# Optimization experiments

Hardware: AMD Instinct MI355X
Metric: run time of the kernel (lower is better)

Reference implementation:

```python
import jax, jax.numpy as jnp
import numpy as np

Nw, Nt, IN_DIM, OUT_DIM, H, FEAT = 200000, 20000, 128, 256, 8, 64
DH = OUT_DIM // H
DEG = 32
E = Nt * DEG
FFN = 512
NEG_SLOPE = 0.01  # F.leaky_relu default


def setup_inputs() -> dict:
    key = jax.random.key(0)
    ks = jax.random.split(key, 12)
    w = jax.random.normal(ks[0], (Nw, IN_DIM), jnp.float32)
    t = jax.random.normal(ks[1], (Nt, OUT_DIM), jnp.float32)
    topic_feat = jax.random.normal(ks[2], (Nt, FEAT), jnp.float32)
    edge_src = jax.random.randint(ks[3], (E,), 0, Nw)
    # every topic node gets exactly DEG in-edges (sorted dst, no empty segments)
    edge_dst = jnp.repeat(jnp.arange(Nt), DEG)
    s = lambda k, sh, f: jax.random.normal(k, sh, jnp.float32) * np.float32(f)
    fc_w = s(ks[4], (H, IN_DIM, DH), 1.0 / np.sqrt(IN_DIM))
    attn_a = s(ks[5], (H, 2 * DH), 1.0 / np.sqrt(2 * DH))
    dstfeat_w = s(ks[6], (H, FEAT, DH), 1.0 / np.sqrt(FEAT))
    proj_w = s(ks[7], (2 * OUT_DIM, OUT_DIM), 1.0 / np.sqrt(2 * OUT_DIM))
    proj_b = jnp.zeros((OUT_DIM,), jnp.float32)
    ffn_w1 = s(ks[8], (OUT_DIM, FFN), 1.0 / np.sqrt(OUT_DIM))
    ffn_b1 = jnp.zeros((FFN,), jnp.float32)
    ffn_w2 = s(ks[9], (FFN, OUT_DIM), 1.0 / np.sqrt(FFN))
    ffn_b2 = jnp.zeros((OUT_DIM,), jnp.float32)
    ln_scale = jnp.ones((OUT_DIM,), jnp.float32)
    ln_bias = jnp.zeros((OUT_DIM,), jnp.float32)
    return dict(w=w, t=t, topic_feat=topic_feat, edge_src=edge_src, edge_dst=edge_dst,
                fc_w=fc_w, attn_a=attn_a, dstfeat_w=dstfeat_w, proj_w=proj_w, proj_b=proj_b,
                ffn_w1=ffn_w1, ffn_b1=ffn_b1, ffn_w2=ffn_w2, ffn_b2=ffn_b2,
                ln_scale=ln_scale, ln_bias=ln_bias)


def reference(w, t, topic_feat, edge_src, edge_dst, fc_w, attn_a, dstfeat_w,
              proj_w, proj_b, ffn_w1, ffn_b1, ffn_w2, ffn_b2, ln_scale, ln_bias):
    # per-head projections: z on word (src) nodes, dstfeat on topic (dst) nodes
    z = jnp.einsum('ni,hid->hnd', w, fc_w)              # [H, Nw, DH]
    dz = jnp.einsum('nf,hfd->hnd', topic_feat, dstfeat_w)  # [H, Nt, DH]
    # attn_fc(cat(z_src, dstfeat)) decomposes into per-node dot products
    s_src = jnp.einsum('hnd,hd->hn', z, attn_a[:, :DH])   # [H, Nw]
    s_dst = jnp.einsum('hnd,hd->hn', dz, attn_a[:, DH:])  # [H, Nt]
    e = s_src[:, edge_src] + s_dst[:, edge_dst]           # [H, E]
    e = jnp.where(e >= 0, e, NEG_SLOPE * e)               # leaky_relu
    # segment softmax over incoming edges of each dst node (DGL mailbox softmax)
    seg_max = jax.vmap(lambda v: jax.ops.segment_max(v, edge_dst, num_segments=Nt))(e)
    seg_max = jnp.where(jnp.isfinite(seg_max), seg_max, 0.0)  # guard empty segments
    p = jnp.exp(e - seg_max[:, edge_dst])
    denom = jax.vmap(lambda v: jax.ops.segment_sum(v, edge_dst, num_segments=Nt))(p)
    alpha = p / jnp.maximum(denom[:, edge_dst], 1e-9)     # [H, E]
    msg = alpha[:, :, None] * z[:, edge_src, :]           # [H, E, DH]
    agg = jax.vmap(lambda m: jax.ops.segment_sum(m, edge_dst, num_segments=Nt))(msg)  # [H, Nt, DH]
    h = jnp.transpose(agg, (1, 0, 2)).reshape(Nt, OUT_DIM)  # head concat
    h = jax.nn.elu(h)
    h = jnp.concatenate([h, t], axis=-1) @ proj_w + proj_b  # [Nt, OUT_DIM]
    # PositionwiseFeedForward: LN -> gelu -> linear -> residual (dropout off in eval)
    mu = jnp.mean(h, axis=-1, keepdims=True)
    var = jnp.var(h, axis=-1, keepdims=True)
    xn = (h - mu) / jnp.sqrt(var + 1e-6) * ln_scale + ln_bias
    inter = jax.nn.gelu(xn @ ffn_w1 + ffn_b1, approximate=False)
    return (inter @ ffn_w2 + ffn_b2) + h
```

## Files before the change

### kernel.cpp

```cpp
#include <hip/hip_runtime.h>
#include <hip/hip_bf16.h>

typedef __attribute__((ext_vector_type(8))) short short8v;
typedef __attribute__((ext_vector_type(4))) float f32x4;

#define NW 200000
#define NT 20000
#define KIN 128
#define ODIM 256
#define NH 8
#define DH_ 32
#define FEAT_ 64
#define DEG_ 32
#define FFN_ 512

#define WS_Z     0ull
#define WS_SSRC  102400000ull
#define WS_SDST  108800000ull
#define WS_TBF   119680000ull
#define WS_B1T   129920000ull
#define WS_PWT   129985536ull
#define WS_W1T   130247680ull
#define WS_W2T   130509824ull
#define WS_ABT   130771968ull


__device__ __forceinline__ unsigned short f2bf(float x) {
    __hip_bfloat16 b = __float2bfloat16(x);
    return *reinterpret_cast<unsigned short*>(&b);
}
__device__ __forceinline__ float bf2f(unsigned short u) {
    unsigned int v = ((unsigned int)u) << 16;
    return __uint_as_float(v);
}

__global__ __launch_bounds__(256) void prep_w(const float* __restrict__ fc_w,
        const float* __restrict__ proj_w, const float* __restrict__ w1,
        const float* __restrict__ w2, const float* __restrict__ attn_a,
        unsigned short* __restrict__ b1f, unsigned short* __restrict__ pwf,
        unsigned short* __restrict__ w1f, unsigned short* __restrict__ w2f,
        unsigned short* __restrict__ abt) {
    int i = blockIdx.x * 256 + threadIdx.x;
    int j = i & 7, l = (i >> 3) & 63;
    int l16 = l & 15, lq = l >> 4;
    if (i < 32768) {
        int kk = (i >> 9) & 3, g = i >> 11;
        int c = g * 16 + l16, k = kk * 32 + lq * 8 + j;
        int h = c >> 5, d = c & 31;
        b1f[i] = f2bf(fc_w[(h * KIN + k) * DH_ + d]);
    }
    if (i < 4096) {
        int h = i >> 8, p = i & 255;
        int c = (p >> 6) * 64 + (p & 3) * 16 + ((p >> 2) & 15);
        abt[i] = ((c >> 5) == h) ? f2bf(attn_a[h * 64 + (c & 31)]) : (unsigned short)0;
    }
    {
        int kk = (i >> 9) & 15, g = i >> 13;
        int c = g * 16 + l16, k = kk * 32 + lq * 8 + j;
        int kp = k;
        if (k < 256)
            kp = ((k >> 6) << 6) + (k & 3) * 16 + ((k >> 2) & 15);
        pwf[i] = f2bf(proj_w[(size_t)kp * ODIM + c]);
    }
    {
        int kk = (i >> 9) & 7, g = i >> 12;
        int c = g * 16 + l16, k = kk * 32 + lq * 8 + j;
        w1f[i] = f2bf(w1[(size_t)k * FFN_ + c]);
    }
    {
        int kk = (i >> 9) & 15, g = i >> 13;
        int c = g * 16 + l16, k = kk * 32 + lq * 8 + j;
        w2f[i] = f2bf(w2[(size_t)k * ODIM + c]);
    }
}

__global__ __launch_bounds__(256) void prep_t(const float* __restrict__ t,
                                              unsigned short* __restrict__ tbf) {
    int i = blockIdx.x * 256 + threadIdx.x;
    const float4* p = (const float4*)(t + (size_t)i * 8);
    float4 a = p[0], b = p[1];
    short8v o;
    o[0] = (short)f2bf(a.x); o[1] = (short)f2bf(a.y);
    o[2] = (short)f2bf(a.z); o[3] = (short)f2bf(a.w);
    o[4] = (short)f2bf(b.x); o[5] = (short)f2bf(b.y);
    o[6] = (short)f2bf(b.z); o[7] = (short)f2bf(b.w);
    *((short8v*)tbf + i) = o;
}

#define ZRP 264
#define TPB 5
__global__ __launch_bounds__(256) void k1_z(const float* __restrict__ w,
        const unsigned short* __restrict__ b1f, const unsigned short* __restrict__ abt,
        unsigned short* __restrict__ z, float* __restrict__ s_src) {
    __shared__ unsigned short aS[2][64 * 136];
    __shared__ unsigned short zR[64 * ZRP];
    const int tid = threadIdx.x;
    const int wv = tid >> 6, l = tid & 63;
    const int l16 = l & 15, lq = l >> 4;
    const int tile0 = blockIdx.x * TPB;
    float4 vb[8];
    #pragma unroll
    for (int j = 0; j < 8; ++j) {
        int i = tid + j * 256;
        int r = i >> 5, kq = i & 31;
        vb[j] = *(const float4*)(w + (size_t)(tile0 * 64 + r) * KIN + kq * 4);
    }
    #pragma unroll
    for (int j = 0; j < 8; ++j) {
        int i = tid + j * 256;
        int r = i >> 5, kq = i & 31;
        ushort4 u;
        u.x = f2bf(vb[j].x); u.y = f2bf(vb[j].y);
        u.z = f2bf(vb[j].z); u.w = f2bf(vb[j].w);
        *(ushort4*)(&aS[0][r * 136 + kq * 4]) = u;
    }
    for (int t = 0; t < TPB; ++t) {
        const int cur = t & 1;
        const int row0 = (tile0 + t) * 64;
        if (t < TPB - 1) {
            #pragma unroll
            for (int j = 0; j < 8; ++j) {
                int i = tid + j * 256;
                int r = i >> 5, kq = i & 31;
                vb[j] = *(const float4*)(w + (size_t)(row0 + 64 + r) * KIN + kq * 4);
            }
        }
        __syncthreads();
        f32x4 acc[4][4];
        #pragma unroll
        for (int a = 0; a < 4; ++a)
            #pragma unroll
            for (int b = 0; b < 4; ++b)
                acc[a][b] = (f32x4){0.f, 0.f, 0.f, 0.f};
        #pragma unroll
        for (int kk = 0; kk < 4; ++kk) {
            short8v af[4], bfr[4];
            #pragma unroll
            for (int rf = 0; rf < 4; ++rf)
                af[rf] = *(const short8v*)(&aS[cur][(rf * 16 + l16) * 136 + kk * 32 + lq * 8]);
            #pragma unroll
            for (int cf = 0; cf < 4; ++cf)
                bfr[cf] = *(const short8v*)((const short*)b1f +
                            ((((wv * 4 + cf) * 4 + kk) << 9) + l * 8));
            #pragma unroll
            for (int rf = 0; rf < 4; ++rf)
                #pragma unroll
                for (int cf = 0; cf < 4; ++cf)
                    acc[rf][cf] = __builtin_amdgcn_mfma_f32_16x16x32_bf16(
                        af[rf], bfr[cf], acc[rf][cf], 0, 0, 0);
        }
        #pragma unroll
        for (int rl = 0; rl < 4; ++rl)
            #pragma unroll
            for (int q = 0; q < 4; ++q) {
                int row = rl * 16 + lq * 4 + q;
                ushort4 u;
                u.x = f2bf(acc[rl][0][q]); u.y = f2bf(acc[rl][1][q]);
                u.z = f2bf(acc[rl][2][q]); u.w = f2bf(acc[rl][3][q]);
                *(ushort4*)(&zR[row * ZRP + wv * 64 + l16 * 4]) = u;
            }
        __syncthreads();
        {
            const int base = wv * 16;
            f32x4 sacc = (f32x4){0.f, 0.f, 0.f, 0.f};
            #pragma unroll
            for (int kk = 0; kk < 8; ++kk) {
                short8v a = *(const short8v*)(&zR[(base + l16) * ZRP + kk * 32 + lq * 8]);
                short8v b = *(const short8v*)((const short*)abt + (size_t)l16 * 256 + kk * 32 + lq * 8);
                sacc = __builtin_amdgcn_mfma_f32_16x16x32_bf16(a, b, sacc, 0, 0, 0);
            }
            if (l16 < NH) {
                #pragma unroll
                for (int q = 0; q < 4; ++q)
                    s_src[(size_t)(row0 + base + lq * 4 + q) * NH + l16] = sacc[q];
            }
        }
        #pragma unroll
        for (int j = 0; j < 8; ++j) {
            int idx = tid + j * 256;
            int r = idx >> 5, ch = idx & 31;
            short8v v = *(const short8v*)(&zR[r * ZRP + ch * 8]);
            *(short8v*)(z + (size_t)(row0 + r) * ODIM + ch * 8) = v;
        }
        if (t < TPB - 1) {
            #pragma unroll
            for (int j = 0; j < 8; ++j) {
                int i = tid + j * 256;
                int r = i >> 5, kq = i & 31;
                ushort4 u;
                u.x = f2bf(vb[j].x); u.y = f2bf(vb[j].y);
                u.z = f2bf(vb[j].z); u.w = f2bf(vb[j].w);
                *(ushort4*)(&aS[cur ^ 1][r * 136 + kq * 4]) = u;
            }
        }
    }
}

__global__ __launch_bounds__(256) void k_sdst(const float* __restrict__ topic_feat,
        const float* __restrict__ dstfeat_w, const float* __restrict__ attn_a,
        float* __restrict__ s_dst) {
    __shared__ float rS[NH * 65];
    __shared__ float tfS[32 * 65];
    const int tid = threadIdx.x;
    for (int i = tid; i < NH * FEAT_; i += 256) {
        int h = i >> 6, f = i & 63;
        const float* dw = dstfeat_w + (size_t)(h * FEAT_ + f) * DH_;
        const float* aa = attn_a + h * 64 + DH_;
        float s = 0.f;
        #pragma unroll
        for (int d = 0; d < DH_; ++d) s += dw[d] * aa[d];
        rS[h * 65 + f] = s;
    }
    const int n0 = blockIdx.x * 32;
    for (int i = tid; i < 32 * FEAT_; i += 256) {
        int n = i >> 6, f = i & 63;
        tfS[n * 65 + f] = topic_feat[(size_t)(n0 + n) * FEAT_ + f];
    }
    __syncthreads();
    int n = tid >> 3, h = tid & 7;
    float s = 0.f;
    #pragma unroll
    for (int f = 0; f < FEAT_; ++f) s += tfS[n * 65 + f] * rS[h * 65 + f];
    s_dst[(size_t)(n0 + n) * NH + h] = s;
}

#define BUFP 524
#define XNP  268
__global__ __launch_bounds__(256, 3) void k234(const int* __restrict__ edge_src,
        const float* __restrict__ s_src, const float* __restrict__ s_dst,
        const unsigned short* __restrict__ z, const unsigned short* __restrict__ tbf,
        const unsigned short* __restrict__ pwf, const float* __restrict__ proj_b,
        const float* __restrict__ ln_scale, const float* __restrict__ ln_bias,
        const unsigned short* __restrict__ w1f, const float* __restrict__ b1,
        const unsigned short* __restrict__ w2f, const float* __restrict__ b2,
        float* __restrict__ out) {
    __shared__ __align__(16) unsigned short buf[32 * BUFP];
    __shared__ __align__(16) unsigned short xnS[32 * XNP];
    __shared__ float lnP[4][32], lnQ[4][32];
    __shared__ float muS[32], rsS[32];
    const int tid = threadIdx.x;
    const int row0 = blockIdx.x * 32;
    const int wv = tid >> 6, l = tid & 63;
    const int l16 = l & 15, lq = l >> 4;
    const int l8 = l * 8;
    #pragma unroll
    for (int j = 0; j < 8; ++j) {
        int i = tid + j * 256;
        int r = i >> 6, cq = i & 63;
        ushort4 tv = *(const ushort4*)(tbf + (size_t)(row0 + r) * ODIM + cq * 4);
        *(ushort4*)(&buf[r * BUFP + 256 + cq * 4]) = tv;
    }
    {
        float* alphaW = (float*)xnS + wv * 1024;
        const int e32 = l & 31, h0 = (l >> 5) * 4;
        const int half = l >> 5, cl = l & 31;
        const int h0a = (cl >> 3) * 2;
        #pragma unroll
        for (int g = 0; g < 2; ++g) {
            int srcv[4];
            #pragma unroll
            for (int nd = 0; nd < 4; ++nd)
                srcv[nd] = edge_src[(size_t)(row0 + wv * 8 + g * 4 + nd) * DEG_ + e32];
            #pragma unroll
            for (int nd = 0; nd < 4; ++nd) {
                const int n = row0 + wv * 8 + g * 4 + nd;
                float4 ss = *(const float4*)(s_src + (size_t)srcv[nd] * NH + h0);
                float4 sd = *(const float4*)(s_dst + (size_t)n * NH + h0);
                float v[4] = {ss.x + sd.x, ss.y + sd.y, ss.z + sd.z, ss.w + sd.w};
                #pragma unroll
                for (int j = 0; j < 4; ++j) v[j] = (v[j] >= 0.f) ? v[j] : 0.01f * v[j];
                float al[4];
                #pragma unroll
                for (int j = 0; j < 4; ++j) {
                    float m = v[j];
                    #pragma unroll
                    for (int off = 16; off >= 1; off >>= 1)
                        m = fmaxf(m, __shfl_xor(m, off));
                    float p = expf(v[j] - m);
                    float su = p;
                    #pragma unroll
                    for (int off = 16; off >= 1; off >>= 1)
                        su += __shfl_xor(su, off);
                    al[j] = p / fmaxf(su, 1e-9f);
                }
                float4 a4 = {al[0], al[1], al[2], al[3]};
                *(float4*)(&alphaW[nd * 256 + e32 * 8 + h0]) = a4;
            }
            asm volatile("s_waitcnt lgkmcnt(0)" ::: "memory");
            #pragma unroll
            for (int nd = 0; nd < 4; ++nd) {
                const int r = wv * 8 + g * 4 + nd;
                float acc[8];
                #pragma unroll
                for (int j = 0; j < 8; ++j) acc[j] = 0.f;
                #pragma unroll 4
                for (int ee = 0; ee < 16; ++ee) {
                    int e = ee * 2 + half;
                    int sp = __shfl(srcv[nd], e);
                    float a_lo = alphaW[nd * 256 + e * 8 + h0a];
                    float a_hi = alphaW[nd * 256 + e * 8 + h0a + 1];
                    short8v zv = *(const short8v*)(z + (size_t)sp * ODIM + cl * 8);
                    #pragma unroll
                    for (int u = 0; u < 8; ++u) {
                        float a = ((u >> 1) & 1) ? a_hi : a_lo;
                        acc[u] += a * bf2f((unsigned short)zv[u]);
                    }
                }
                #pragma unroll
                for (int j = 0; j < 8; ++j)
                    acc[j] += __shfl_xor(acc[j], 32);
                if (half == 0) {
                    ushort4 o0, o1;
                    float v0 = (acc[0] > 0.f) ? acc[0] : expm1f(acc[0]);
                    float v1 = (acc[1] > 0.f) ? acc[1] : expm1f(acc[1]);
                    float v2 = (acc[2] > 0.f) ? acc[2] : expm1f(acc[2]);
                    float v3 = (acc[3] > 0.f) ? acc[3] : expm1f(acc[3]);
                    float v4 = (acc[4] > 0.f) ? acc[4] : expm1f(acc[4]);
                    float v5 = (acc[5] > 0.f) ? acc[5] : expm1f(acc[5]);
                    float v6 = (acc[6] > 0.f) ? acc[6] : expm1f(acc[6]);
                    float v7 = (acc[7] > 0.f) ? acc[7] : expm1f(acc[7]);
                    o0.x = f2bf(v0); o0.y = f2bf(v1); o0.z = f2bf(v2); o0.w = f2bf(v3);
                    o1.x = f2bf(v4); o1.y = f2bf(v5); o1.z = f2bf(v6); o1.w = f2bf(v7);
                    *(ushort4*)(&buf[r * BUFP + cl * 8]) = o0;
                    *(ushort4*)(&buf[r * BUFP + cl * 8 + 4]) = o1;
                }
            }
        }
    }
    __syncthreads();
    f32x4 acc0[2][4];
    #pragma unroll
    for (int rf = 0; rf < 2; ++rf)
        #pragma unroll
        for (int cf = 0; cf < 4; ++cf) acc0[rf][cf] = (f32x4){0.f, 0.f, 0.f, 0.f};
    {
        short8v bp[2][4];
        #pragma unroll
        for (int cf = 0; cf < 4; ++cf)
            bp[0][cf] = *(const short8v*)((const short*)pwf + ((((wv * 4 + cf) * 16) << 9) + l8));
        #pragma unroll
        for (int kk = 0; kk < 16; ++kk) {
            const int cur = kk & 1;
            if (kk < 15) {
                #pragma unroll
                for (int cf = 0; cf < 4; ++cf)
                    bp[cur ^ 1][cf] = *(const short8v*)((const short*)pwf +
                        ((((wv * 4 + cf) * 16 + kk + 1) << 9) + l8));
            }
            short8v a0 = *(const short8v*)(&buf[l16 * BUFP + kk * 32 + lq * 8]);
            short8v a1 = *(const short8v*)(&buf[(16 + l16) * BUFP + kk * 32 + lq * 8]);
            #pragma unroll
            for (int cf = 0; cf < 4; ++cf) {
                acc0[0][cf] = __builtin_amdgcn_mfma_f32_16x16x32_bf16(a0, bp[cur][cf], acc0[0][cf], 0, 0, 0);
                acc0[1][cf] = __builtin_amdgcn_mfma_f32_16x16x32_bf16(a1, bp[cur][cf], acc0[1][cf], 0, 0, 0);
            }
        }
    }
    #pragma unroll
    for (int cf = 0; cf < 4; ++cf) {
        float bb = proj_b[wv * 64 + cf * 16 + l16];
        #pragma unroll
        for (int rf = 0; rf < 2; ++rf)
            #pragma unroll
            for (int q = 0; q < 4; ++q) acc0[rf][cf][q] += bb;
    }
    #pragma unroll
    for (int rf = 0; rf < 2; ++rf)
        #pragma unroll
        for (int q = 0; q < 4; ++q) {
            float s = 0.f, s2 = 0.f;
            #pragma unroll
            for (int cf = 0; cf < 4; ++cf) {
                float v = acc0[rf][cf][q];
                s += v; s2 += v * v;
            }
            s  += __shfl_xor(s, 1);  s2 += __shfl_xor(s2, 1);
            s  += __shfl_xor(s, 2);  s2 += __shfl_xor(s2, 2);
            s  += __shfl_xor(s, 4);  s2 += __shfl_xor(s2, 4);
            s  += __shfl_xor(s, 8);  s2 += __shfl_xor(s2, 8);
            if (l16 == 0) {
                int row = rf * 16 + lq * 4 + q;
                lnP[wv][row] = s; lnQ[wv][row] = s2;
            }
        }
    __syncthreads();
    if (tid < 32) {
        float s = lnP[0][tid] + lnP[1][tid] + lnP[2][tid] + lnP[3][tid];
        float s2 = lnQ[0][tid] + lnQ[1][tid] + lnQ[2][tid] + lnQ[3][tid];
        float mu = s * (1.f / 256.f);
        float var = s2 * (1.f / 256.f) - mu * mu;
        muS[tid] = mu;
        rsS[tid] = rsqrtf(var + 1e-6f);
    }
    __syncthreads();
    #pragma unroll
    for (int cf = 0; cf < 4; ++cf) {
        int c = wv * 64 + cf * 16 + l16;
        float ls = ln_scale[c], lb = ln_bias[c];
        #pragma unroll
        for (int rf = 0; rf < 2; ++rf)
            #pragma unroll
            for (int q = 0; q < 4; ++q) {
                int row = rf * 16 + lq * 4 + q;
                float x = (acc0[rf][cf][q] - muS[row]) * rsS[row] * ls + lb;
                xnS[row * XNP + c] = f2bf(x);
            }
    }
    __syncthreads();
    {
        f32x4 acc1[2][8];
        #pragma unroll
        for (int rf = 0; rf < 2; ++rf)
            #pragma unroll
            for (int cf = 0; cf < 8; ++cf) acc1[rf][cf] = (f32x4){0.f, 0.f, 0.f, 0.f};
        #pragma unroll 2
        for (int kk = 0; kk < 8; ++kk) {
            short8v a0 = *(const short8v*)(&xnS[l16 * XNP + kk * 32 + lq * 8]);
            short8v a1 = *(const short8v*)(&xnS[(16 + l16) * XNP + kk * 32 + lq * 8]);
            #pragma unroll
            for (int cf = 0; cf < 8; ++cf) {
                short8v b = *(const short8v*)((const short*)w1f +
                    ((((wv * 8 + cf) * 8 + kk) << 9) + l8));
                acc1[0][cf] = __builtin_amdgcn_mfma_f32_16x16x32_bf16(a0, b, acc1[0][cf], 0, 0, 0);
                acc1[1][cf] = __builtin_amdgcn_mfma_f32_16x16x32_bf16(a1, b, acc1[1][cf], 0, 0, 0);
            }
        }
        #pragma unroll
        for (int cf = 0; cf < 8; ++cf) {
            int c = wv * 128 + cf * 16 + l16;
            float bb = b1[c];
            #pragma unroll
            for (int rf = 0; rf < 2; ++rf)
                #pragma unroll
                for (int q = 0; q < 4; ++q) {
                    float x = acc1[rf][cf][q] + bb;
                    x = 0.5f * x * (1.f + erff(x * 0.70710678118654752f));
                    buf[(rf * 16 + lq * 4 + q) * BUFP + c] = f2bf(x);
                }
        }
    }
    __syncthreads();
    {
        f32x4 acc2[2][4];
        #pragma unroll
        for (int rf = 0; rf < 2; ++rf)
            #pragma unroll
            for (int cf = 0; cf < 4; ++cf) acc2[rf][cf] = (f32x4){0.f, 0.f, 0.f, 0.f};
        short8v bp[2][4];
        #pragma unroll
        for (int cf = 0; cf < 4; ++cf)
            bp[0][cf] = *(const short8v*)((const short*)w2f + ((((wv * 4 + cf) * 16) << 9) + l8));
        #pragma unroll
        for (int kk = 0; kk < 16; ++kk) {
            const int cur = kk & 1;
            if (kk < 15) {
                #pragma unroll
                for (int cf = 0; cf < 4; ++cf)
                    bp[cur ^ 1][cf] = *(const short8v*)((const short*)w2f +
                        ((((wv * 4 + cf) * 16 + kk + 1) << 9) + l8));
            }
            short8v a0 = *(const short8v*)(&buf[l16 * BUFP + kk * 32 + lq * 8]);
            short8v a1 = *(const short8v*)(&buf[(16 + l16) * BUFP + kk * 32 + lq * 8]);
            #pragma unroll
            for (int cf = 0; cf < 4; ++cf) {
                acc2[0][cf] = __builtin_amdgcn_mfma_f32_16x16x32_bf16(a0, bp[cur][cf], acc2[0][cf], 0, 0, 0);
                acc2[1][cf] = __builtin_amdgcn_mfma_f32_16x16x32_bf16(a1, bp[cur][cf], acc2[1][cf], 0, 0, 0);
            }
        }
        #pragma unroll
        for (int cf = 0; cf < 4; ++cf) {
            int c = wv * 64 + cf * 16 + l16;
            float bb = b2[c];
            #pragma unroll
            for (int rf = 0; rf < 2; ++rf)
                #pragma unroll
                for (int q = 0; q < 4; ++q) {
                    int row = rf * 16 + lq * 4 + q;
                    out[(size_t)(row0 + row) * ODIM + c] =
                        acc2[rf][cf][q] + bb + acc0[rf][cf][q];
                }
        }
    }
}

extern "C" void kernel_launch(void* const* d_in, const int* in_sizes, int n_in,
                              void* d_out, int out_size, void* d_ws, size_t ws_size,
                              hipStream_t stream) {
    const float* w          = (const float*)d_in[0];
    const float* t          = (const float*)d_in[1];
    const float* topic_feat = (const float*)d_in[2];
    const int*   edge_src   = (const int*)d_in[3];
    const float* fc_w       = (const float*)d_in[5];
    const float* attn_a     = (const float*)d_in[6];
    const float* dstfeat_w  = (const float*)d_in[7];
    const float* proj_w     = (const float*)d_in[8];
    const float* proj_b     = (const float*)d_in[9];
    const float* ffn_w1     = (const float*)d_in[10];
    const float* ffn_b1     = (const float*)d_in[11];
    const float* ffn_w2     = (const float*)d_in[12];
    const float* ffn_b2     = (const float*)d_in[13];
    const float* ln_scale   = (const float*)d_in[14];
    const float* ln_bias    = (const float*)d_in[15];
    float* out = (float*)d_out;

    char* ws = (char*)d_ws;
    unsigned short* z    = (unsigned short*)(ws + WS_Z);
    float* s_src         = (float*)(ws + WS_SSRC);
    float* s_dst         = (float*)(ws + WS_SDST);
    unsigned short* tbf  = (unsigned short*)(ws + WS_TBF);
    unsigned short* b1f  = (unsigned short*)(ws + WS_B1T);
    unsigned short* pwf  = (unsigned short*)(ws + WS_PWT);
    unsigned short* w1f  = (unsigned short*)(ws + WS_W1T);
    unsigned short* w2f  = (unsigned short*)(ws + WS_W2T);
    unsigned short* abt  = (unsigned short*)(ws + WS_ABT);

    hipLaunchKernelGGL(prep_w, dim3(512),           dim3(256), 0, stream,
                       fc_w, proj_w, ffn_w1, ffn_w2, attn_a, b1f, pwf, w1f, w2f, abt);
    hipLaunchKernelGGL(prep_t, dim3(2500),          dim3(256), 0, stream, t, tbf);
    hipLaunchKernelGGL(k1_z,   dim3(NW / (64*TPB)), dim3(256), 0, stream,
                       w, b1f, abt, z, s_src);
    hipLaunchKernelGGL(k_sdst, dim3(NT / 32),       dim3(256), 0, stream,
                       topic_feat, dstfeat_w, attn_a, s_dst);
    hipLaunchKernelGGL(k234,   dim3(NT / 32),       dim3(256), 0, stream,
                       edge_src, s_src, s_dst, z, tbf, pwf, proj_b,
                       ln_scale, ln_bias, w1f, ffn_b1, w2f, ffn_b2, out);
}
```

Baseline: 171.7 us.

## Halve rows per block in fused aggregation/FFN kernel to raise occupancy

The fused gather/attention/projection/FFN kernel now processes 16 topic rows per block instead of 32. The grid doubles, the MFMA row-fragment dimension drops from two to one, and the launch bound rises to 4 waves per SIMD. This cuts accumulator registers and shared buffer size so more blocks can be resident to hide the latency of the irregular z gathers. The cost is that each block reloads the full bf16 weight matrices for only half as many rows, doubling weight traffic and giving each MFMA step less reuse of each B fragment.

```diff
diff --git a/kernel.cpp b/kernel.cpp
--- a/kernel.cpp
+++ b/kernel.cpp
@@ -226,7 +226,7 @@
 
 #define BUFP 524
 #define XNP  268
-__global__ __launch_bounds__(256, 3) void k234(const int* __restrict__ edge_src,
+__global__ __launch_bounds__(256, 4) void k234(const int* __restrict__ edge_src,
         const float* __restrict__ s_src, const float* __restrict__ s_dst,
         const unsigned short* __restrict__ z, const unsigned short* __restrict__ tbf,
         const unsigned short* __restrict__ pwf, const float* __restrict__ proj_b,
@@ -234,17 +234,17 @@
         const unsigned short* __restrict__ w1f, const float* __restrict__ b1,
         const unsigned short* __restrict__ w2f, const float* __restrict__ b2,
         float* __restrict__ out) {
-    __shared__ __align__(16) unsigned short buf[32 * BUFP];
+    __shared__ __align__(16) unsigned short buf[16 * BUFP];
     __shared__ __align__(16) unsigned short xnS[32 * XNP];
-    __shared__ float lnP[4][32], lnQ[4][32];
-    __shared__ float muS[32], rsS[32];
+    __shared__ float lnP[4][16], lnQ[4][16];
+    __shared__ float muS[16], rsS[16];
     const int tid = threadIdx.x;
-    const int row0 = blockIdx.x * 32;
+    const int row0 = blockIdx.x * 16;
     const int wv = tid >> 6, l = tid & 63;
     const int l16 = l & 15, lq = l >> 4;
     const int l8 = l * 8;
     #pragma unroll
-    for (int j = 0; j < 8; ++j) {
+    for (int j = 0; j < 4; ++j) {
         int i = tid + j * 256;
         int r = i >> 6, cq = i & 63;
         ushort4 tv = *(const ushort4*)(tbf + (size_t)(row0 + r) * ODIM + cq * 4);
@@ -255,84 +255,79 @@
         const int e32 = l & 31, h0 = (l >> 5) * 4;
         const int half = l >> 5, cl = l & 31;
         const int h0a = (cl >> 3) * 2;
-        #pragma unroll
-        for (int g = 0; g < 2; ++g) {
-            int srcv[4];
-            #pragma unroll
-            for (int nd = 0; nd < 4; ++nd)
-                srcv[nd] = edge_src[(size_t)(row0 + wv * 8 + g * 4 + nd) * DEG_ + e32];
-            #pragma unroll
-            for (int nd = 0; nd < 4; ++nd) {
-                const int n = row0 + wv * 8 + g * 4 + nd;
-                float4 ss = *(const float4*)(s_src + (size_t)srcv[nd] * NH + h0);
-                float4 sd = *(const float4*)(s_dst + (size_t)n * NH + h0);
-                float v[4] = {ss.x + sd.x, ss.y + sd.y, ss.z + sd.z, ss.w + sd.w};
-                #pragma unroll
-                for (int j = 0; j < 4; ++j) v[j] = (v[j] >= 0.f) ? v[j] : 0.01f * v[j];
-                float al[4];
-                #pragma unroll
-                for (int j = 0; j < 4; ++j) {
-                    float m = v[j];
-                    #pragma unroll
-                    for (int off = 16; off >= 1; off >>= 1)
-                        m = fmaxf(m, __shfl_xor(m, off));
-                    float p = expf(v[j] - m);
-                    float su = p;
-                    #pragma unroll
-                    for (int off = 16; off >= 1; off >>= 1)
-                        su += __shfl_xor(su, off);
-                    al[j] = p / fmaxf(su, 1e-9f);
+        int srcv[4];
+        #pragma unroll
+        for (int nd = 0; nd < 4; ++nd)
+            srcv[nd] = edge_src[(size_t)(row0 + wv * 4 + nd) * DEG_ + e32];
+        #pragma unroll
+        for (int nd = 0; nd < 4; ++nd) {
+            const int n = row0 + wv * 4 + nd;
+            float4 ss = *(const float4*)(s_src + (size_t)srcv[nd] * NH + h0);
+            float4 sd = *(const float4*)(s_dst + (size_t)n * NH + h0);
+            float v[4] = {ss.x + sd.x, ss.y + sd.y, ss.z + sd.z, ss.w + sd.w};
+            #pragma unroll
+            for (int j = 0; j < 4; ++j) v[j] = (v[j] >= 0.f) ? v[j] : 0.01f * v[j];
+            float al[4];
+            #pragma unroll
+            for (int j = 0; j < 4; ++j) {
+                float m = v[j];
+                #pragma unroll
+                for (int off = 16; off >= 1; off >>= 1)
+                    m = fmaxf(m, __shfl_xor(m, off));
+                float p = expf(v[j] - m);
+                float su = p;
+                #pragma unroll
+                for (int off = 16; off >= 1; off >>= 1)
+                    su += __shfl_xor(su, off);
+                al[j] = p / fmaxf(su, 1e-9f);
+            }
+            float4 a4 = {al[0], al[1], al[2], al[3]};
+            *(float4*)(&alphaW[nd * 256 + e32 * 8 + h0]) = a4;
+        }
+        asm volatile("s_waitcnt lgkmcnt(0)" ::: "memory");
+        #pragma unroll
+        for (int nd = 0; nd < 4; ++nd) {
+            const int r = wv * 4 + nd;
+            float acc[8];
+            #pragma unroll
+            for (int j = 0; j < 8; ++j) acc[j] = 0.f;
+            #pragma unroll 4
+            for (int ee = 0; ee < 16; ++ee) {
+                int e = ee * 2 + half;
+                int sp = __shfl(srcv[nd], e);
+                float a_lo = alphaW[nd * 256 + e * 8 + h0a];
+                float a_hi = alphaW[nd * 256 + e * 8 + h0a + 1];
+                short8v zv = *(const short8v*)(z + (size_t)sp * ODIM + cl * 8);
+                #pragma unroll
+                for (int u = 0; u < 8; ++u) {
+                    float a = ((u >> 1) & 1) ? a_hi : a_lo;
+                    acc[u] += a * bf2f((unsigned short)zv[u]);
                 }
-                float4 a4 = {al[0], al[1], al[2], al[3]};
-                *(float4*)(&alphaW[nd * 256 + e32 * 8 + h0]) = a4;
-            }
-            asm volatile("s_waitcnt lgkmcnt(0)" ::: "memory");
-            #pragma unroll
-            for (int nd = 0; nd < 4; ++nd) {
-                const int r = wv * 8 + g * 4 + nd;
-                float acc[8];
-                #pragma unroll
-                for (int j = 0; j < 8; ++j) acc[j] = 0.f;
-                #pragma unroll 4
-                for (int ee = 0; ee < 16; ++ee) {
-                    int e = ee * 2 + half;
-                    int sp = __shfl(srcv[nd], e);
-                    float a_lo = alphaW[nd * 256 + e * 8 + h0a];
-                    float a_hi = alphaW[nd * 256 + e * 8 + h0a + 1];
-                    short8v zv = *(const short8v*)(z + (size_t)sp * ODIM + cl * 8);
-                    #pragma unroll
-                    for (int u = 0; u < 8; ++u) {
-                        float a = ((u >> 1) & 1) ? a_hi : a_lo;
-                        acc[u] += a * bf2f((unsigned short)zv[u]);
-                    }
-                }
-                #pragma unroll
-                for (int j = 0; j < 8; ++j)
-                    acc[j] += __shfl_xor(acc[j], 32);
-                if (half == 0) {
-                    ushort4 o0, o1;
-                    float v0 = (acc[0] > 0.f) ? acc[0] : expm1f(acc[0]);
-                    float v1 = (acc[1] > 0.f) ? acc[1] : expm1f(acc[1]);
-                    float v2 = (acc[2] > 0.f) ? acc[2] : expm1f(acc[2]);
-                    float v3 = (acc[3] > 0.f) ? acc[3] : expm1f(acc[3]);
-                    float v4 = (acc[4] > 0.f) ? acc[4] : expm1f(acc[4]);
-                    float v5 = (acc[5] > 0.f) ? acc[5] : expm1f(acc[5]);
-                    float v6 = (acc[6] > 0.f) ? acc[6] : expm1f(acc[6]);
-                    float v7 = (acc[7] > 0.f) ? acc[7] : expm1f(acc[7]);
-                    o0.x = f2bf(v0); o0.y = f2bf(v1); o0.z = f2bf(v2); o0.w = f2bf(v3);
-                    o1.x = f2bf(v4); o1.y = f2bf(v5); o1.z = f2bf(v6); o1.w = f2bf(v7);
-                    *(ushort4*)(&buf[r * BUFP + cl * 8]) = o0;
-                    *(ushort4*)(&buf[r * BUFP + cl * 8 + 4]) = o1;
-                }
-            }
-        }
-    }
-    __syncthreads();
-    f32x4 acc0[2][4];
-    #pragma unroll
-    for (int rf = 0; rf < 2; ++rf)
-        #pragma unroll
-        for (int cf = 0; cf < 4; ++cf) acc0[rf][cf] = (f32x4){0.f, 0.f, 0.f, 0.f};
+            }
+            #pragma unroll
+            for (int j = 0; j < 8; ++j)
+                acc[j] += __shfl_xor(acc[j], 32);
+            if (half == 0) {
+                ushort4 o0, o1;
+                float v0 = (acc[0] > 0.f) ? acc[0] : expm1f(acc[0]);
+                float v1 = (acc[1] > 0.f) ? acc[1] : expm1f(acc[1]);
+                float v2 = (acc[2] > 0.f) ? acc[2] : expm1f(acc[2]);
+                float v3 = (acc[3] > 0.f) ? acc[3] : expm1f(acc[3]);
+                float v4 = (acc[4] > 0.f) ? acc[4] : expm1f(acc[4]);
+                float v5 = (acc[5] > 0.f) ? acc[5] : expm1f(acc[5]);
+                float v6 = (acc[6] > 0.f) ? acc[6] : expm1f(acc[6]);
+                float v7 = (acc[7] > 0.f) ? acc[7] : expm1f(acc[7]);
+                o0.x = f2bf(v0); o0.y = f2bf(v1); o0.z = f2bf(v2); o0.w = f2bf(v3);
+                o1.x = f2bf(v4); o1.y = f2bf(v5); o1.z = f2bf(v6); o1.w = f2bf(v7);
+                *(ushort4*)(&buf[r * BUFP + cl * 8]) = o0;
+                *(ushort4*)(&buf[r * BUFP + cl * 8 + 4]) = o1;
+            }
+        }
+    }
+    __syncthreads();
+    f32x4 acc0[4];
+    #pragma unroll
+    for (int cf = 0; cf < 4; ++cf) acc0[cf] = (f32x4){0.f, 0.f, 0.f, 0.f};
     {
         short8v bp[2][4];
         #pragma unroll
@@ -348,43 +343,36 @@
                         ((((wv * 4 + cf) * 16 + kk + 1) << 9) + l8));
             }
             short8v a0 = *(const short8v*)(&buf[l16 * BUFP + kk * 32 + lq * 8]);
-            short8v a1 = *(const short8v*)(&buf[(16 + l16) * BUFP + kk * 32 + lq * 8]);
-            #pragma unroll
-            for (int cf = 0; cf < 4; ++cf) {
-                acc0[0][cf] = __builtin_amdgcn_mfma_f32_16x16x32_bf16(a0, bp[cur][cf], acc0[0][cf], 0, 0, 0);
-                acc0[1][cf] = __builtin_amdgcn_mfma_f32_16x16x32_bf16(a1, bp[cur][cf], acc0[1][cf], 0, 0, 0);
-            }
+            #pragma unroll
+            for (int cf = 0; cf < 4; ++cf)
+                acc0[cf] = __builtin_amdgcn_mfma_f32_16x16x32_bf16(a0, bp[cur][cf], acc0[cf], 0, 0, 0);
         }
     }
     #pragma unroll
     for (int cf = 0; cf < 4; ++cf) {
         float bb = proj_b[wv * 64 + cf * 16 + l16];
         #pragma unroll
-        for (int rf = 0; rf < 2; ++rf)
-            #pragma unroll
-            for (int q = 0; q < 4; ++q) acc0[rf][cf][q] += bb;
-    }
-    #pragma unroll
-    for (int rf = 0; rf < 2; ++rf)
-        #pragma unroll
-        for (int q = 0; q < 4; ++q) {
-            float s = 0.f, s2 = 0.f;
-            #pragma unroll
-            for (int cf = 0; cf < 4; ++cf) {
-                float v = acc0[rf][cf][q];
-                s += v; s2 += v * v;
-            }
-            s  += __shfl_xor(s, 1);  s2 += __shfl_xor(s2, 1);
-            s  += __shfl_xor(s, 2);  s2 += __shfl_xor(s2, 2);
-            s  += __shfl_xor(s, 4);  s2 += __shfl_xor(s2, 4);
-            s  += __shfl_xor(s, 8);  s2 += __shfl_xor(s2, 8);
-            if (l16 == 0) {
-                int row = rf * 16 + lq * 4 + q;
-                lnP[wv][row] = s; lnQ[wv][row] = s2;
-            }
-        }
-    __syncthreads();
-    if (tid < 32) {
+        for (int q = 0; q < 4; ++q) acc0[cf][q] += bb;
+    }
+    #pragma unroll
+    for (int q = 0; q < 4; ++q) {
+        float s = 0.f, s2 = 0.f;
+        #pragma unroll
+        for (int cf = 0; cf < 4; ++cf) {
+            float v = acc0[cf][q];
+            s += v; s2 += v * v;
+        }
+        s  += __shfl_xor(s, 1);  s2 += __shfl_xor(s2, 1);
+        s  += __shfl_xor(s, 2);  s2 += __shfl_xor(s2, 2);
+        s  += __shfl_xor(s, 4);  s2 += __shfl_xor(s2, 4);
+        s  += __shfl_xor(s, 8);  s2 += __shfl_xor(s2, 8);
+        if (l16 == 0) {
+            int row = lq * 4 + q;
+            lnP[wv][row] = s; lnQ[wv][row] = s2;
+        }
+    }
+    __syncthreads();
+    if (tid < 16) {
         float s = lnP[0][tid] + lnP[1][tid] + lnP[2][tid] + lnP[3][tid];
         float s2 = lnQ[0][tid] + lnQ[1][tid] + lnQ[2][tid] + lnQ[3][tid];
         float mu = s * (1.f / 256.f);
@@ -398,31 +386,25 @@
         int c = wv * 64 + cf * 16 + l16;
         float ls = ln_scale[c], lb = ln_bias[c];
         #pragma unroll
-        for (int rf = 0; rf < 2; ++rf)
-            #pragma unroll
-            for (int q = 0; q < 4; ++q) {
-                int row = rf * 16 + lq * 4 + q;
-                float x = (acc0[rf][cf][q] - muS[row]) * rsS[row] * ls + lb;
-                xnS[row * XNP + c] = f2bf(x);
-            }
-    }
-    __syncthreads();
-    {
-        f32x4 acc1[2][8];
-        #pragma unroll
-        for (int rf = 0; rf < 2; ++rf)
-            #pragma unroll
-            for (int cf = 0; cf < 8; ++cf) acc1[rf][cf] = (f32x4){0.f, 0.f, 0.f, 0.f};
+        for (int q = 0; q < 4; ++q) {
+            int row = lq * 4 + q;
+            float x = (acc0[cf][q] - muS[row]) * rsS[row] * ls + lb;
+            xnS[row * XNP + c] = f2bf(x);
+        }
+    }
+    __syncthreads();
+    {
+        f32x4 acc1[8];
+        #pragma unroll
+        for (int cf = 0; cf < 8; ++cf) acc1[cf] = (f32x4){0.f, 0.f, 0.f, 0.f};
         #pragma unroll 2
         for (int kk = 0; kk < 8; ++kk) {
             short8v a0 = *(const short8v*)(&xnS[l16 * XNP + kk * 32 + lq * 8]);
-            short8v a1 = *(const short8v*)(&xnS[(16 + l16) * XNP + kk * 32 + lq * 8]);
             #pragma unroll
             for (int cf = 0; cf < 8; ++cf) {
                 short8v b = *(const short8v*)((const short*)w1f +
                     ((((wv * 8 + cf) * 8 + kk) << 9) + l8));
-                acc1[0][cf] = __builtin_amdgcn_mfma_f32_16x16x32_bf16(a0, b, acc1[0][cf], 0, 0, 0);
-                acc1[1][cf] = __builtin_amdgcn_mfma_f32_16x16x32_bf16(a1, b, acc1[1][cf], 0, 0, 0);
+                acc1[cf] = __builtin_amdgcn_mfma_f32_16x16x32_bf16(a0, b, acc1[cf], 0, 0, 0);
             }
         }
         #pragma unroll
@@ -430,22 +412,18 @@
             int c = wv * 128 + cf * 16 + l16;
             float bb = b1[c];
             #pragma unroll
-            for (int rf = 0; rf < 2; ++rf)
-                #pragma unroll
-                for (int q = 0; q < 4; ++q) {
-                    float x = acc1[rf][cf][q] + bb;
-                    x = 0.5f * x * (1.f + erff(x * 0.70710678118654752f));
-                    buf[(rf * 16 + lq * 4 + q) * BUFP + c] = f2bf(x);
-                }
-        }
-    }
-    __syncthreads();
-    {
-        f32x4 acc2[2][4];
-        #pragma unroll
-        for (int rf = 0; rf < 2; ++rf)
-            #pragma unroll
-            for (int cf = 0; cf < 4; ++cf) acc2[rf][cf] = (f32x4){0.f, 0.f, 0.f, 0.f};
+            for (int q = 0; q < 4; ++q) {
+                float x = acc1[cf][q] + bb;
+                x = 0.5f * x * (1.f + erff(x * 0.70710678118654752f));
+                buf[(lq * 4 + q) * BUFP + c] = f2bf(x);
+            }
+        }
+    }
+    __syncthreads();
+    {
+        f32x4 acc2[4];
+        #pragma unroll
+        for (int cf = 0; cf < 4; ++cf) acc2[cf] = (f32x4){0.f, 0.f, 0.f, 0.f};
         short8v bp[2][4];
         #pragma unroll
         for (int cf = 0; cf < 4; ++cf)
@@ -460,25 +438,19 @@
                         ((((wv * 4 + cf) * 16 + kk + 1) << 9) + l8));
             }
             short8v a0 = *(const short8v*)(&buf[l16 * BUFP + kk * 32 + lq * 8]);
-            short8v a1 = *(const short8v*)(&buf[(16 + l16) * BUFP + kk * 32 + lq * 8]);
-            #pragma unroll
-            for (int cf = 0; cf < 4; ++cf) {
-                acc2[0][cf] = __builtin_amdgcn_mfma_f32_16x16x32_bf16(a0, bp[cur][cf], acc2[0][cf], 0, 0, 0);
-                acc2[1][cf] = __builtin_amdgcn_mfma_f32_16x16x32_bf16(a1, bp[cur][cf], acc2[1][cf], 0, 0, 0);
-            }
+            #pragma unroll
+            for (int cf = 0; cf < 4; ++cf)
+                acc2[cf] = __builtin_amdgcn_mfma_f32_16x16x32_bf16(a0, bp[cur][cf], acc2[cf], 0, 0, 0);
         }
         #pragma unroll
         for (int cf = 0; cf < 4; ++cf) {
             int c = wv * 64 + cf * 16 + l16;
             float bb = b2[c];
             #pragma unroll
-            for (int rf = 0; rf < 2; ++rf)
-                #pragma unroll
-                for (int q = 0; q < 4; ++q) {
-                    int row = rf * 16 + lq * 4 + q;
-                    out[(size_t)(row0 + row) * ODIM + c] =
-                        acc2[rf][cf][q] + bb + acc0[rf][cf][q];
-                }
+            for (int q = 0; q < 4; ++q) {
+                int row = lq * 4 + q;
+                out[(size_t)(row0 + row) * ODIM + c] = acc2[cf][q] + bb + acc0[cf][q];
+            }
         }
     }
 }
@@ -521,7 +493,7 @@
                        w, b1f, abt, z, s_src);
     hipLaunchKernelGGL(k_sdst, dim3(NT / 32),       dim3(256), 0, stream,
                        topic_feat, dstfeat_w, attn_a, s_dst);
-    hipLaunchKernelGGL(k234,   dim3(NT / 32),       dim3(256), 0, stream,
+    hipLaunchKernelGGL(k234,   dim3(NT / 16),       dim3(256), 0, stream,
                        edge_src, s_src, s_dst, z, tbf, pwf, proj_b,
                        ln_scale, ln_bias, w1f, ffn_b1, w2f, ffn_b2, out);
 }
```

Measured after the change: 192.4 us. 12.0% more time.
